# Kernel tuning notes

Measured on AMD Instinct MI355X. Metric: run time of the kernel, lower is better.

Reference implementation:

```python
import jax, jax.numpy as jnp
import numpy as np

DIM = 2048
D_INNER = 4096
D_STATE = 128
N_GROUPS = 1
N_HEADS = 32
D_CONV = 4
CHUNK = 256
CONV_DIM = D_INNER + 2 * N_GROUPS * D_STATE  # 4352
D_IN_PROJ = 2 * D_INNER + 2 * N_GROUPS * D_STATE + N_HEADS  # 8480
EPS = 1e-5
BATCH, SEQ = 2, 2048


def setup_inputs() -> dict:
    key = jax.random.key(0)
    ks = jax.random.split(key, 8)
    inputs = jax.random.normal(ks[0], (BATCH, SEQ, DIM), jnp.float32)
    in_proj_w = jax.random.normal(ks[1], (D_IN_PROJ, DIM), jnp.float32) / np.sqrt(DIM)
    in_proj_b = jnp.zeros((D_IN_PROJ,), jnp.float32)
    out_proj_w = jax.random.normal(ks[2], (DIM, D_INNER), jnp.float32) / np.sqrt(D_INNER)
    out_proj_b = jnp.zeros((DIM,), jnp.float32)
    conv_w = jax.random.uniform(ks[3], (CONV_DIM, 1, D_CONV), jnp.float32)
    conv_b = jnp.zeros((CONV_DIM,), jnp.float32)
    # dt_bias = inv-softplus of dt sampled log-uniform in [dt_min, dt_max]
    dt = jnp.exp(jax.random.uniform(ks[4], (N_HEADS,), jnp.float32) * (np.log(0.1) - np.log(0.001)) + np.log(0.001))
    dt = jnp.clip(dt, 1e-4, None)
    dt_bias = dt + jnp.log(-jnp.expm1(-dt))
    A_log = jnp.log(jax.random.uniform(ks[5], (N_HEADS,), jnp.float32, 1e-3, 16.0))
    D = jnp.ones((N_HEADS,), jnp.float32)
    norm_w = jnp.ones((D_INNER,), jnp.float32)
    return {"inputs": inputs, "in_proj_w": in_proj_w, "in_proj_b": in_proj_b,
            "out_proj_w": out_proj_w, "out_proj_b": out_proj_b,
            "conv_w": conv_w, "conv_b": conv_b, "dt_bias": dt_bias,
            "A_log": A_log, "D": D, "norm_w": norm_w}


def segsum(x):
    # x: (..., T) -> (..., T, T); segsum[l, s] = sum_{i=s+1..l} x[i] for l>=s, else -inf
    T = x.shape[-1]
    cs = jnp.cumsum(x, axis=-1)
    seg = cs[..., :, None] - cs[..., None, :]
    mask = jnp.tril(jnp.ones((T, T), bool))
    return jnp.where(mask, seg, -jnp.inf)


def chunk_scan(x, dt, A, B, C, chunk, D):
    # x: (b,s,h,p)  dt: (b,s,h)  A: (h,)  B,C: (b,s,g,n)  D: (h,)
    b, s, h, p = x.shape
    g, n = B.shape[-2:]
    c = s // chunk
    X = (x * dt[..., None]).reshape(b, c, chunk, h, p)          # bclhp
    Ac = (A * dt).reshape(b, c, chunk, h).transpose(0, 3, 1, 2)  # bhcl
    Bc = B.reshape(b, c, chunk, g, n)
    Cc = C.reshape(b, c, chunk, g, n)
    A_cumsum = jnp.cumsum(Ac, axis=-1)                           # bhcl
    L = jnp.exp(segsum(Ac))                                      # bhcls
    Y_diag = jnp.einsum('bclgn,bcsgn,bhcls,bcshp->bclhp', Cc, Bc, L, X)
    decay_states = jnp.exp(A_cumsum[..., -1:] - A_cumsum)        # bhcl
    states = jnp.einsum('bclgn,bhcl,bclhp->bcghpn', Bc, decay_states, X)
    states = jnp.concatenate([jnp.zeros_like(states[:, :1]), states], axis=1)
    chunk_sums = jnp.pad(A_cumsum[..., -1], ((0, 0), (0, 0), (1, 0)))  # bh(c+1)
    decay_chunk = jnp.exp(segsum(chunk_sums))                    # bh(c+1)(c+1)
    new_states = jnp.einsum('bhzc,bcghpn->bzghpn', decay_chunk, states)
    states = new_states[:, :-1]
    state_decay_out = jnp.exp(A_cumsum)
    Y_off = jnp.einsum('bclgn,bcghpn,bhcl->bclhp', Cc, states, state_decay_out)
    Y = (Y_diag + Y_off).reshape(b, s, h, p)
    return Y + D[None, None, :, None] * x


def reference(inputs, in_proj_w, in_proj_b, out_proj_w, out_proj_b,
              conv_w, conv_b, dt_bias, A_log, D, norm_w):
    b, s, _ = inputs.shape
    A = -jnp.exp(A_log)
    zxbcdt = inputs @ in_proj_w.T + in_proj_b                     # (b,s,D_IN_PROJ)
    z = zxbcdt[..., :D_INNER]
    xBC = zxbcdt[..., D_INNER:D_INNER + CONV_DIM]
    dt = zxbcdt[..., D_INNER + CONV_DIM:]
    dt = jax.nn.softplus(dt + dt_bias)
    # causal depthwise conv1d (left pad D_CONV-1, truncate to seqlen)
    xpad = jnp.pad(xBC, ((0, 0), (D_CONV - 1, 0), (0, 0)))
    conv = conv_b
    for k in range(D_CONV):
        conv = conv + xpad[:, k:k + s, :] * conv_w[:, 0, k]
    xBC = jax.nn.silu(conv)
    x = xBC[..., :D_INNER].reshape(b, s, N_HEADS, D_INNER // N_HEADS)
    B = xBC[..., D_INNER:D_INNER + N_GROUPS * D_STATE].reshape(b, s, N_GROUPS, D_STATE)
    C = xBC[..., D_INNER + N_GROUPS * D_STATE:].reshape(b, s, N_GROUPS, D_STATE)
    y = chunk_scan(x, dt, A, B, C, CHUNK, D).reshape(b, s, D_INNER)
    y = y * jax.nn.silu(z)
    y = y * jax.lax.rsqrt(jnp.mean(y * y, axis=-1, keepdims=True) + EPS) * norm_w
    return y @ out_proj_w.T + out_proj_b
```

## Files before the change

### kernel.cpp

```cpp
#include <hip/hip_runtime.h>
#include <math.h>

#define DIMM 2048
#define D_INNER 4096
#define D_STATE 128
#define N_HEADS 32
#define CHUNK 256
#define CONV_DIM 4352
#define D_IN_PROJ 8480
#define BATCH 2
#define SEQ 2048
#define NTOK 4096
#define NCHUNK 8
#define HEADDIM 128
#define NXB 4480

typedef short bf16x8 __attribute__((ext_vector_type(8)));
typedef float f32x4 __attribute__((ext_vector_type(4)));

__device__ __forceinline__ unsigned short f32_to_bf16(float f) {
    unsigned int u = __float_as_uint(f);
    unsigned int r = (u + 0x7FFFu + ((u >> 16) & 1u)) >> 16;
    return (unsigned short)r;
}
__device__ __forceinline__ float bf16_to_f32(unsigned short h) {
    return __uint_as_float(((unsigned int)h) << 16);
}
__device__ __forceinline__ float siluf(float v) { return v / (1.f + expf(-v)); }

__device__ __forceinline__ void gload_lds16(const unsigned short* g, unsigned short* l) {
    __builtin_amdgcn_global_load_lds(
        (const __attribute__((address_space(1))) unsigned int*)((const void*)g),
        (__attribute__((address_space(3))) unsigned int*)((void*)l),
        16, 0, 0);
}

__global__ __launch_bounds__(256)
void gemm_bt(const unsigned short* __restrict__ A, long lda, long sAb, long sAc, long sAh,
             const unsigned short* __restrict__ Wg, long ldw, long sWb, long sWc, long sWh,
             void* __restrict__ Cmv, long ldc, long sCb, long sCc, long sCh,
             int K, int nc, int nh,
             const float* __restrict__ bias, int bias_n,
             const float* __restrict__ kscale, long sKb, long sKc, long sKh,
             const float* __restrict__ nscale, long sNb, long sNc, long sNh,
             const float* __restrict__ mscale, long sMb, long sMc, long sMh,
             int accum, int outbf)
{
    __shared__ unsigned short As[128 * 64];
    __shared__ unsigned short Ws[128 * 64];

    const int tid = threadIdx.x;
    const int z = blockIdx.z;
    const int h = z % nh;
    const int zc = z / nh;
    const int c = zc % nc;
    const int b = zc / nc;

    const unsigned short* Ab = A + (size_t)(b * sAb + c * sAc + h * sAh);
    const unsigned short* Wb = Wg + (size_t)(b * sWb + c * sWc + h * sWh);
    const size_t coff = (size_t)(b * sCb + c * sCc + h * sCh);
    const float* ksb = kscale ? (kscale + (size_t)(b * sKb + c * sKc + h * sKh)) : nullptr;
    const float* nsb = nscale ? (nscale + (size_t)(b * sNb + c * sNc + h * sNh)) : nullptr;
    const float* msb = mscale ? (mscale + (size_t)(b * sMb + c * sMc + h * sMh)) : nullptr;

    const long bm = (long)blockIdx.y * 128;
    const long bn = (long)blockIdx.x * 128;

    const int lane = tid & 63;
    const int wave = tid >> 6;
    const int wrow = (wave >> 1) * 64;
    const int wcol = (wave & 1) * 64;
    const int lr = lane & 15;
    const int quad = lane >> 4;

    f32x4 acc[4][4] = {};

    for (int k0 = 0; k0 < K; k0 += 64) {
        __syncthreads();
        if (!ksb) {
            #pragma unroll
            for (int q = 0; q < 4; ++q) {
                int cidx = tid + q * 256;
                int row = cidx >> 3;
                int sl = cidx & 7;
                int cg = sl ^ (row & 7);
                gload_lds16(Ab + (bm + row) * lda + k0 + cg * 8, &As[cidx * 8]);
                gload_lds16(Wb + (bn + row) * ldw + k0 + cg * 8, &Ws[cidx * 8]);
            }
        } else {
            #pragma unroll
            for (int q = 0; q < 4; ++q) {
                int cidx = tid + q * 256;
                int row = cidx >> 3;
                int sl = cidx & 7;
                int cg = sl ^ (row & 7);
                int kk = k0 + cg * 8;
                uint4 va = *(const uint4*)(Ab + (bm + row) * lda + kk);
                const float* ks = ksb + kk;
                unsigned int vv[4] = {va.x, va.y, va.z, va.w};
                #pragma unroll
                for (int e = 0; e < 4; ++e) {
                    float lo = __uint_as_float((vv[e] & 0xFFFFu) << 16) * ks[2 * e];
                    float hi = __uint_as_float(vv[e] & 0xFFFF0000u) * ks[2 * e + 1];
                    vv[e] = (unsigned int)f32_to_bf16(lo) | ((unsigned int)f32_to_bf16(hi) << 16);
                }
                *(uint4*)&As[cidx * 8] = make_uint4(vv[0], vv[1], vv[2], vv[3]);
                uint4 vw = *(const uint4*)(Wb + (bn + row) * ldw + kk);
                *(uint4*)&Ws[cidx * 8] = vw;
            }
        }
        __syncthreads();
        #pragma unroll
        for (int kk = 0; kk < 64; kk += 32) {
            const int cb = (kk >> 3) + quad;
            bf16x8 av[4], bv[4];
            #pragma unroll
            for (int i = 0; i < 4; ++i) {
                int row = wrow + i * 16 + lr;
                av[i] = *(const bf16x8*)&As[row * 64 + ((cb ^ (row & 7)) * 8)];
            }
            #pragma unroll
            for (int j = 0; j < 4; ++j) {
                int row = wcol + j * 16 + lr;
                bv[j] = *(const bf16x8*)&Ws[row * 64 + ((cb ^ (row & 7)) * 8)];
            }
            #pragma unroll
            for (int i = 0; i < 4; ++i)
                #pragma unroll
                for (int j = 0; j < 4; ++j)
                    acc[i][j] = __builtin_amdgcn_mfma_f32_16x16x32_bf16(av[i], bv[j], acc[i][j], 0, 0, 0);
        }
    }

    #pragma unroll
    for (int i = 0; i < 4; ++i) {
        #pragma unroll
        for (int j = 0; j < 4; ++j) {
            #pragma unroll
            for (int r = 0; r < 4; ++r) {
                long row = bm + wrow + i * 16 + quad * 4 + r;
                long col = bn + wcol + j * 16 + lr;
                float v = acc[i][j][r];
                if (msb) v *= msb[row];
                if (nsb) v *= nsb[col];
                if (bias && col < bias_n) v += bias[col];
                if (outbf) {
                    unsigned short* dst = (unsigned short*)Cmv + coff + row * ldc + col;
                    if (accum) v += bf16_to_f32(*dst);
                    *dst = f32_to_bf16(v);
                } else {
                    float* dst = (float*)Cmv + coff + row * ldc + col;
                    if (accum) *dst += v; else *dst = v;
                }
            }
        }
    }
}

__global__ __launch_bounds__(256)
void k_convert(const float* __restrict__ src, unsigned short* __restrict__ dst,
               long ncopy, long ntotal)
{
    long i = (long)blockIdx.x * 256 + threadIdx.x;
    long stride = (long)gridDim.x * 256;
    for (; i < ntotal; i += stride)
        dst[i] = (i < ncopy) ? f32_to_bf16(src[i]) : (unsigned short)0;
}

__global__ __launch_bounds__(256)
void k_dt(const unsigned short* __restrict__ Zx, const float* __restrict__ dt_bias,
          float* __restrict__ dtv)
{
    int i = blockIdx.x * 256 + threadIdx.x;
    if (i >= NTOK * N_HEADS) return;
    int t = i >> 5, h = i & 31;
    float raw = bf16_to_f32(Zx[(size_t)t * NXB + CONV_DIM + h]) + dt_bias[h];
    dtv[i] = raw > 20.f ? raw : log1pf(expf(raw));
}

__global__ __launch_bounds__(256)
void k_cumsum(const float* __restrict__ dtv, const float* __restrict__ A_log,
              float* __restrict__ Acs, float* __restrict__ cdec,
              float* __restrict__ eacs, float* __restrict__ ctot)
{
    int z = blockIdx.x;
    int h = z & 31, c = (z >> 5) & 7, b = z >> 8;
    int l = threadIdx.x;
    int t = ((b * 8 + c) << 8) + l;
    float dv = dtv[t * 32 + h];
    float a = -expf(A_log[h]) * dv;
    __shared__ float sb[256];
    sb[l] = a;
    __syncthreads();
    float v = a;
    for (int o = 1; o < 256; o <<= 1) {
        float add = (l >= o) ? sb[l - o] : 0.f;
        __syncthreads();
        v += add;
        sb[l] = v;
        __syncthreads();
    }
    float total = sb[255];
    Acs[(size_t)z * 256 + l] = v;
    cdec[(size_t)z * 256 + l] = expf(total - v) * dv;
    eacs[(size_t)z * 256 + l] = expf(v);
    if (l == 255) ctot[(b * 32 + h) * 8 + c] = total;
}

__global__ __launch_bounds__(256)
void k_conv(const unsigned short* __restrict__ Zx, const float* __restrict__ conv_w,
            const float* __restrict__ conv_b, const float* __restrict__ Dv,
            unsigned short* __restrict__ Xt, unsigned short* __restrict__ Y,
            unsigned short* __restrict__ Bbf, unsigned short* __restrict__ Cbf,
            unsigned short* __restrict__ Bt)
{
    __shared__ unsigned short In[68 * 64];
    __shared__ unsigned short OutL[64 * 65];

    const int c0 = blockIdx.x * 64;
    const int s0 = blockIdx.y * 64;
    const int b  = blockIdx.z;
    const int tid = threadIdx.x;

    for (int i = tid; i < 68 * 64; i += 256) {
        int j = i >> 6, c = i & 63;
        int sg = s0 + j - 3;
        unsigned short v = 0;
        if (sg >= 0 && j < 67) v = Zx[(size_t)((b << 11) + sg) * NXB + c0 + c];
        In[i] = v;
    }
    __syncthreads();

    const int cl = tid & 63;
    const int ch = c0 + cl;
    const float w0 = conv_w[ch * 4 + 0], w1 = conv_w[ch * 4 + 1];
    const float w2 = conv_w[ch * 4 + 2], w3 = conv_w[ch * 4 + 3];
    const float cb = conv_b[ch];
    #pragma unroll
    for (int it = 0; it < 16; ++it) {
        int sl = (tid >> 6) + it * 4;
        float a = cb
            + bf16_to_f32(In[(sl + 0) * 64 + cl]) * w0
            + bf16_to_f32(In[(sl + 1) * 64 + cl]) * w1
            + bf16_to_f32(In[(sl + 2) * 64 + cl]) * w2
            + bf16_to_f32(In[(sl + 3) * 64 + cl]) * w3;
        OutL[cl * 65 + sl] = f32_to_bf16(siluf(a));
    }
    __syncthreads();

    if (c0 < D_INNER + D_STATE) {
        for (int i = tid; i < 4096; i += 256) {
            int cr = i >> 6, sc = i & 63;
            unsigned short v = OutL[cr * 65 + sc];
            int ch2 = c0 + cr;
            if (ch2 < D_INNER) {
                int hh = ch2 >> 7, p = ch2 & 127;
                Xt[((size_t)(b * 32 + hh) * 128 + p) * 2048 + s0 + sc] = v;
            } else {
                int n = ch2 - D_INNER;
                Bt[((size_t)(b * 128 + n)) * 2048 + s0 + sc] = v;
            }
        }
    }
    for (int i = tid; i < 4096; i += 256) {
        int sr = i >> 6, cc = i & 63;
        int t = (b << 11) + s0 + sr;
        int ch2 = c0 + cc;
        unsigned short v = OutL[cc * 65 + sr];
        if (ch2 < D_INNER) {
            Y[(size_t)t * 4096 + ch2] = f32_to_bf16(Dv[ch2 >> 7] * bf16_to_f32(v));
        } else if (ch2 < D_INNER + D_STATE) {
            Bbf[(size_t)t * 128 + (ch2 - D_INNER)] = v;
        } else {
            Cbf[(size_t)t * 128 + (ch2 - D_INNER - D_STATE)] = v;
        }
    }
}

__global__ __launch_bounds__(256)
void k_wbuild(const float* __restrict__ Acs, const float* __restrict__ dtv,
              const float* __restrict__ G, unsigned short* __restrict__ Wbf,
              int z_base)
{
    int l = blockIdx.x;
    int zr = blockIdx.y;
    int z = z_base + zr;
    int s = threadIdx.x;
    int h = z & 31, c = (z >> 5) & 7, b = z >> 8;
    float w = 0.f;
    if (s <= l) {
        float e = expf(Acs[(size_t)z * 256 + l] - Acs[(size_t)z * 256 + s]);
        int t = ((b * 8 + c) << 8) + s;
        w = e * dtv[t * 32 + h] * G[(size_t)(b * 8 + c) * 65536 + l * 256 + s];
    }
    Wbf[(size_t)zr * 65536 + l * 256 + s] = f32_to_bf16(w);
}

__global__ __launch_bounds__(256)
void k_recur(const float* __restrict__ Sloc, const float* __restrict__ ctot,
             unsigned short* __restrict__ Sin)
{
    int i = blockIdx.x * 256 + threadIdx.x;
    int n = i & 127, p = (i >> 7) & 127, h = (i >> 14) & 31, b = i >> 19;
    float s = 0.f;
    for (int c = 0; c < 8; ++c) {
        size_t idx = ((((size_t)(b * 8 + c) * 32 + h) * 128 + p) * 128 + n);
        Sin[idx] = f32_to_bf16(s);
        s = s * expf(ctot[(b * 32 + h) * 8 + c]) + Sloc[idx];
    }
}

__global__ __launch_bounds__(256)
void k_combine(const unsigned short* __restrict__ Y, const unsigned short* __restrict__ Zz,
               const float* __restrict__ norm_w, unsigned short* __restrict__ Ybf)
{
    int t = blockIdx.x;
    int tid = threadIdx.x;
    const unsigned int* Yr = (const unsigned int*)(Y + (size_t)t * 4096);
    const unsigned int* Zr = (const unsigned int*)(Zz + (size_t)t * 4096);
    float vals[16];
    float ss = 0.f;
    #pragma unroll
    for (int it = 0; it < 8; ++it) {
        int j = tid + it * 256;
        unsigned int y2 = Yr[j], z2 = Zr[j];
        float y0 = __uint_as_float((y2 & 0xFFFFu) << 16);
        float y1 = __uint_as_float(y2 & 0xFFFF0000u);
        float z0 = __uint_as_float((z2 & 0xFFFFu) << 16);
        float z1 = __uint_as_float(z2 & 0xFFFF0000u);
        y0 *= siluf(z0);
        y1 *= siluf(z1);
        vals[2 * it] = y0;
        vals[2 * it + 1] = y1;
        ss += y0 * y0 + y1 * y1;
    }
    #pragma unroll
    for (int o = 32; o > 0; o >>= 1) ss += __shfl_down(ss, o, 64);
    __shared__ float red[4];
    if ((tid & 63) == 0) red[tid >> 6] = ss;
    __syncthreads();
    float tot = red[0] + red[1] + red[2] + red[3];
    float scale = rsqrtf(tot / 4096.f + 1e-5f);
    unsigned int* Yw = (unsigned int*)(Ybf + (size_t)t * 4096);
    #pragma unroll
    for (int it = 0; it < 8; ++it) {
        int j = tid + it * 256;
        unsigned short o0 = f32_to_bf16(vals[2 * it] * scale * norm_w[2 * j]);
        unsigned short o1 = f32_to_bf16(vals[2 * it + 1] * scale * norm_w[2 * j + 1]);
        Yw[j] = (unsigned int)o0 | ((unsigned int)o1 << 16);
    }
}

extern "C" void kernel_launch(void* const* d_in, const int* in_sizes, int n_in,
                              void* d_out, int out_size, void* d_ws, size_t ws_size,
                              hipStream_t stream)
{
    if (n_in < 11) return;
    const float* inputs     = (const float*)d_in[0];
    const float* in_proj_w  = (const float*)d_in[1];
    const float* in_proj_b  = (const float*)d_in[2];
    const float* out_proj_w = (const float*)d_in[3];
    const float* out_proj_b = (const float*)d_in[4];
    const float* conv_w     = (const float*)d_in[5];
    const float* conv_b     = (const float*)d_in[6];
    const float* dt_bias    = (const float*)d_in[7];
    const float* A_log      = (const float*)d_in[8];
    const float* Dv         = (const float*)d_in[9];
    const float* norm_w     = (const float*)d_in[10];
    float* out = (float*)d_out;

    char* base = (char*)d_ws;
    const size_t SZ_ABF  = (size_t)NTOK * DIMM * 2;
    const size_t SZ_W1   = (size_t)8576 * DIMM * 2;
    const size_t SZ_R0   = SZ_ABF + SZ_W1;
    const size_t SZ_ZZ   = (size_t)NTOK * 4096 * 2;
    const size_t SZ_R3   = (size_t)NTOK * NXB * 2;
    const size_t SZ_XT   = (size_t)BATCH * 32 * 128 * 2048 * 2;
    const size_t SZ_R2   = (size_t)256 * 65536 * 2;
    size_t off = 0;
    char* R0   = base + off; off += SZ_R0;
    char* Zz   = base + off; off += SZ_ZZ;
    char* R3   = base + off; off += SZ_R3;
    char* XtB  = base + off; off += SZ_XT;
    char* R2   = base + off; off += SZ_R2;
    unsigned short* Bbf = (unsigned short*)(base + off); off += (size_t)NTOK * 128 * 2;
    unsigned short* Cbf = (unsigned short*)(base + off); off += (size_t)NTOK * 128 * 2;
    unsigned short* Bt  = (unsigned short*)(base + off); off += (size_t)BATCH * 128 * 2048 * 2;
    float* dtv  = (float*)(base + off); off += (size_t)NTOK * 32 * 4;
    float* Acs  = (float*)(base + off); off += (size_t)512 * 256 * 4;
    float* cdec = (float*)(base + off); off += (size_t)512 * 256 * 4;
    float* eacs = (float*)(base + off); off += (size_t)512 * 256 * 4;
    float* ctot = (float*)(base + off); off += (size_t)512 * 4;
    float* G    = (float*)(base + off); off += (size_t)16 * 65536 * 4;
    if (off > ws_size) return;

    unsigned short* Abf  = (unsigned short*)R0;
    unsigned short* W1bf = (unsigned short*)(R0 + SZ_ABF);
    unsigned short* Sin  = (unsigned short*)R0;
    unsigned short* Y    = (unsigned short*)(R0 + SZ_ABF);
    unsigned short* Zzb  = (unsigned short*)Zz;
    unsigned short* Zxb  = (unsigned short*)R3;
    unsigned short* Ybf  = (unsigned short*)R3;
    unsigned short* Xt   = (unsigned short*)XtB;
    unsigned short* Wbf  = (unsigned short*)R2;
    unsigned short* W2bf = (unsigned short*)R2;
    float* Sloc = (float*)d_out;

    k_convert<<<2048, 256, 0, stream>>>(inputs, Abf, (long)NTOK * DIMM, (long)NTOK * DIMM);
    k_convert<<<2048, 256, 0, stream>>>(in_proj_w, W1bf, (long)D_IN_PROJ * DIMM, (long)8576 * DIMM);

    gemm_bt<<<dim3(32, 32, 1), 256, 0, stream>>>(
        Abf, DIMM, 0, 0, 0,  W1bf, DIMM, 0, 0, 0,
        Zzb, 4096, 0, 0, 0,  DIMM, 1, 1,
        in_proj_b, 4096,  nullptr, 0, 0, 0,  nullptr, 0, 0, 0,  nullptr, 0, 0, 0,  0, 1);
    gemm_bt<<<dim3(35, 32, 1), 256, 0, stream>>>(
        Abf, DIMM, 0, 0, 0,  W1bf + (size_t)4096 * DIMM, DIMM, 0, 0, 0,
        Zxb, NXB, 0, 0, 0,  DIMM, 1, 1,
        in_proj_b + 4096, D_IN_PROJ - 4096,  nullptr, 0, 0, 0,  nullptr, 0, 0, 0,
        nullptr, 0, 0, 0,  0, 1);

    k_dt<<<(NTOK * N_HEADS) / 256, 256, 0, stream>>>(Zxb, dt_bias, dtv);
    k_cumsum<<<512, 256, 0, stream>>>(dtv, A_log, Acs, cdec, eacs, ctot);

    k_conv<<<dim3(68, 32, 2), 256, 0, stream>>>(Zxb, conv_w, conv_b, Dv, Xt, Y, Bbf, Cbf, Bt);

    gemm_bt<<<dim3(2, 2, 16), 256, 0, stream>>>(
        Cbf, 128, 2048L * 128, 256L * 128, 0,
        Bbf, 128, 2048L * 128, 256L * 128, 0,
        G, 256, 8L * 65536, 65536, 0,
        128, 8, 1,
        nullptr, 0, nullptr, 0, 0, 0, nullptr, 0, 0, 0, nullptr, 0, 0, 0, 0, 0);

    for (int s = 0; s < 2; ++s) {
        k_wbuild<<<dim3(256, 256, 1), 256, 0, stream>>>(Acs, dtv, G, Wbf, s * 256);
        gemm_bt<<<dim3(1, 2, 256), 256, 0, stream>>>(
            Wbf, 256, 0, 32L * 65536, 65536,
            Xt + (size_t)s * 32 * 128 * 2048, 2048, 0, 256, 128L * 2048,
            Y + (size_t)s * 2048 * 4096, 4096, 0, 256L * 4096, 128,
            256, 8, 32,
            nullptr, 0,
            nullptr, 0, 0, 0,  nullptr, 0, 0, 0,  nullptr, 0, 0, 0,
            1, 1);
    }

    gemm_bt<<<dim3(1, 1, 512), 256, 0, stream>>>(
        Xt, 2048, 32L * 128 * 2048, 256, 128L * 2048,
        Bt, 2048, 128L * 2048, 256, 0,
        Sloc, 128, 8L * 32 * 16384, 32L * 16384, 16384,
        256, 8, 32,
        nullptr, 0,
        cdec, 8L * 32 * 256, 32L * 256, 256,
        nullptr, 0, 0, 0,  nullptr, 0, 0, 0,
        0, 0);

    k_recur<<<4096, 256, 0, stream>>>(Sloc, ctot, Sin);

    gemm_bt<<<dim3(1, 2, 512), 256, 0, stream>>>(
        Cbf, 128, 2048L * 128, 256L * 128, 0,
        Sin, 128, 8L * 32 * 16384, 32L * 16384, 16384,
        Y, 4096, 2048L * 4096, 256L * 4096, 128,
        128, 8, 32,
        nullptr, 0,
        nullptr, 0, 0, 0,  nullptr, 0, 0, 0,
        eacs, 8L * 32 * 256, 32L * 256, 256,
        1, 1);

    k_convert<<<2048, 256, 0, stream>>>(out_proj_w, W2bf, (long)DIMM * D_INNER, (long)DIMM * D_INNER);

    k_combine<<<NTOK, 256, 0, stream>>>(Y, Zzb, norm_w, Ybf);

    gemm_bt<<<dim3(16, 32, 1), 256, 0, stream>>>(
        Ybf, D_INNER, 0, 0, 0,
        W2bf, D_INNER, 0, 0, 0,
        out, DIMM, 0, 0, 0,
        D_INNER, 1, 1,
        out_proj_b, DIMM,
        nullptr, 0, 0, 0,  nullptr, 0, 0, 0,  nullptr, 0, 0, 0,
        0, 0);
}
```

Baseline: 775.2 us.

## Swizzle GEMM tile order, vectorize conversion, fuse softplus dt into cumsum

The GEMM kernel now remaps its linear block id into bands of up to eight M-tiles, walking N-tiles within each band so concurrently running blocks share A and W tiles in L2. The fp32-to-bf16 conversion kernel now handles four elements per thread with float4 loads and ushort4 stores. The separate dt softplus kernel is folded into the cumsum kernel, which removes one launch and one round trip of dtv through memory. The swizzle only changes which tile each block computes, so correctness depends on the band math covering every tile exactly once.

Result: no change. 765.3 us (-1.3%).

```diff
diff --git a/kernel.cpp b/kernel.cpp
--- a/kernel.cpp
+++ b/kernel.cpp
@@ -56,6 +56,16 @@
     const int c = zc % nc;
     const int b = zc / nc;
 
+    const int tilesN = gridDim.x, tilesM = gridDim.y;
+    int bid = (int)blockIdx.y * tilesN + (int)blockIdx.x;
+    const int band = (tilesM < 8) ? tilesM : 8;
+    const int per = band * tilesN;
+    int g = bid / per;
+    int r = bid % per;
+    int rows = tilesM - g * band; if (rows > band) rows = band;
+    int mt = g * band + (r % rows);
+    int nt = r / rows;
+
     const unsigned short* Ab = A + (size_t)(b * sAb + c * sAc + h * sAh);
     const unsigned short* Wb = Wg + (size_t)(b * sWb + c * sWc + h * sWh);
     const size_t coff = (size_t)(b * sCb + c * sCc + h * sCh);
@@ -63,8 +73,8 @@
     const float* nsb = nscale ? (nscale + (size_t)(b * sNb + c * sNc + h * sNh)) : nullptr;
     const float* msb = mscale ? (mscale + (size_t)(b * sMb + c * sMc + h * sMh)) : nullptr;
 
-    const long bm = (long)blockIdx.y * 128;
-    const long bn = (long)blockIdx.x * 128;
+    const long bm = (long)mt * 128;
+    const long bn = (long)nt * 128;
 
     const int lane = tid & 63;
     const int wave = tid >> 6;
@@ -137,10 +147,10 @@
         #pragma unroll
         for (int j = 0; j < 4; ++j) {
             #pragma unroll
-            for (int r = 0; r < 4; ++r) {
-                long row = bm + wrow + i * 16 + quad * 4 + r;
+            for (int r2 = 0; r2 < 4; ++r2) {
+                long row = bm + wrow + i * 16 + quad * 4 + r2;
                 long col = bn + wcol + j * 16 + lr;
-                float v = acc[i][j][r];
+                float v = acc[i][j][r2];
                 if (msb) v *= msb[row];
                 if (nsb) v *= nsb[col];
                 if (bias && col < bias_n) v += bias[col];
@@ -161,33 +171,38 @@
 void k_convert(const float* __restrict__ src, unsigned short* __restrict__ dst,
                long ncopy, long ntotal)
 {
-    long i = (long)blockIdx.x * 256 + threadIdx.x;
-    long stride = (long)gridDim.x * 256;
-    for (; i < ntotal; i += stride)
-        dst[i] = (i < ncopy) ? f32_to_bf16(src[i]) : (unsigned short)0;
-}
-
-__global__ __launch_bounds__(256)
-void k_dt(const unsigned short* __restrict__ Zx, const float* __restrict__ dt_bias,
-          float* __restrict__ dtv)
-{
-    int i = blockIdx.x * 256 + threadIdx.x;
-    if (i >= NTOK * N_HEADS) return;
-    int t = i >> 5, h = i & 31;
-    float raw = bf16_to_f32(Zx[(size_t)t * NXB + CONV_DIM + h]) + dt_bias[h];
-    dtv[i] = raw > 20.f ? raw : log1pf(expf(raw));
-}
-
-__global__ __launch_bounds__(256)
-void k_cumsum(const float* __restrict__ dtv, const float* __restrict__ A_log,
-              float* __restrict__ Acs, float* __restrict__ cdec,
-              float* __restrict__ eacs, float* __restrict__ ctot)
+    long i4 = ((long)blockIdx.x * 256 + threadIdx.x) * 4;
+    long stride = (long)gridDim.x * 256 * 4;
+    for (; i4 < ntotal; i4 += stride) {
+        ushort4 o;
+        if (i4 + 3 < ncopy) {
+            float4 v = *(const float4*)(src + i4);
+            o.x = f32_to_bf16(v.x); o.y = f32_to_bf16(v.y);
+            o.z = f32_to_bf16(v.z); o.w = f32_to_bf16(v.w);
+        } else {
+            o.x = (i4 + 0 < ncopy) ? f32_to_bf16(src[i4 + 0]) : 0;
+            o.y = (i4 + 1 < ncopy) ? f32_to_bf16(src[i4 + 1]) : 0;
+            o.z = (i4 + 2 < ncopy) ? f32_to_bf16(src[i4 + 2]) : 0;
+            o.w = (i4 + 3 < ncopy) ? f32_to_bf16(src[i4 + 3]) : 0;
+        }
+        *(ushort4*)(dst + i4) = o;
+    }
+}
+
+__global__ __launch_bounds__(256)
+void k_cumsum(const unsigned short* __restrict__ Zx, const float* __restrict__ dt_bias,
+              const float* __restrict__ A_log,
+              float* __restrict__ dtv, float* __restrict__ Acs,
+              float* __restrict__ cdec, float* __restrict__ eacs,
+              float* __restrict__ ctot)
 {
     int z = blockIdx.x;
     int h = z & 31, c = (z >> 5) & 7, b = z >> 8;
     int l = threadIdx.x;
     int t = ((b * 8 + c) << 8) + l;
-    float dv = dtv[t * 32 + h];
+    float raw = bf16_to_f32(Zx[(size_t)t * NXB + CONV_DIM + h]) + dt_bias[h];
+    float dv = raw > 20.f ? raw : log1pf(expf(raw));
+    dtv[t * 32 + h] = dv;
     float a = -expf(A_log[h]) * dv;
     __shared__ float sb[256];
     sb[l] = a;
@@ -419,8 +434,7 @@
         in_proj_b + 4096, D_IN_PROJ - 4096,  nullptr, 0, 0, 0,  nullptr, 0, 0, 0,
         nullptr, 0, 0, 0,  0, 1);
 
-    k_dt<<<(NTOK * N_HEADS) / 256, 256, 0, stream>>>(Zxb, dt_bias, dtv);
-    k_cumsum<<<512, 256, 0, stream>>>(dtv, A_log, Acs, cdec, eacs, ctot);
+    k_cumsum<<<512, 256, 0, stream>>>(Zxb, dt_bias, A_log, dtv, Acs, cdec, eacs, ctot);
 
     k_conv<<<dim3(68, 32, 2), 256, 0, stream>>>(Zxb, conv_w, conv_b, Dv, Xt, Y, Bbf, Cbf, Bt);
 
```
